# Kernel optimization log

Hardware: AMD Instinct MI355X
Metric: run time of the kernel (lower is better)

The kernel has to match this reference:

```python
import math
import jax, jax.numpy as jnp
import numpy as np

NUM_TOKENS = 8192
MODEL_DIM = 1024
NUM_EXPERTS = 64
CAPACITY_FACTOR = 1.0
MIN_CAPACITY = 8
SHIFT_PRIORITY = 0.5
LOAD_BALANCE_W = 0.01


def setup_inputs() -> dict:
    key = jax.random.key(0)
    k1, k2 = jax.random.split(key)
    x = jax.random.normal(k1, (NUM_TOKENS, MODEL_DIM), dtype=jnp.float32)
    # torch.nn.Linear(model_dim, num_experts, bias=False).weight -> [E, D]
    wg_weight = jax.random.normal(k2, (NUM_EXPERTS, MODEL_DIM), dtype=jnp.float32) * 0.02
    return {"x": x, "wg_weight": wg_weight}


def reference(x, wg_weight):
    S = x.shape[0]
    E = wg_weight.shape[0]
    # gate projection (fp32, as in DeepSpeed gating)
    logits = jnp.einsum('sd,ed->se', x, wg_weight)  # [S, E]
    gates = jax.nn.softmax(logits, axis=1)
    original_gates = gates

    # _capacity: ceil(S/E * capacity_factor), clamped to min_capacity (static)
    capacity = max(int(math.ceil(S / E * CAPACITY_FACTOR)), MIN_CAPACITY)

    indices1_s = jnp.argmax(gates, axis=1)                      # [S]
    mask1 = jax.nn.one_hot(indices1_s, E, dtype=jnp.int32)      # [S, E]
    exp_counts = jnp.sum(mask1, axis=0)                         # [E]

    # AuxLoss: GShard load-balance loss, zloss/entropy weights are 0
    me = jnp.mean(gates, axis=0)
    ce = jnp.mean(mask1.astype(gates.dtype), axis=0)
    l_aux = jnp.sum(me * ce) * E * LOAD_BALANCE_W

    # shifted-priority routing: sort tokens by -max_gate, roll, positional cumsum
    importance_scores = -jnp.max(gates, axis=1)                 # [S]
    sort_indices = jnp.argsort(importance_scores)               # [S]
    shift_num = int(S * SHIFT_PRIORITY)                         # static
    sort_indices = jnp.roll(sort_indices, shift_num)
    recover_indices = jnp.argsort(sort_indices)
    sorted_mask1 = mask1[sort_indices]                          # [S, E]
    sorted_cumsum1 = (jnp.cumsum(sorted_mask1, axis=0) - 1) * sorted_mask1
    locations1 = sorted_cumsum1[recover_indices]                # [S, E]

    # capacity dropping
    mask1 = mask1 * (locations1 < capacity).astype(jnp.int32)
    locations1_s = jnp.sum(locations1 * mask1, axis=1)          # [S]

    gates_masked = original_gates * mask1.astype(gates.dtype)   # [S, E]
    locations1_sc = jax.nn.one_hot(locations1_s, capacity, dtype=gates.dtype)  # [S, C]
    combine_weights = jnp.einsum('se,sc->sec', gates_masked, locations1_sc)    # [S, E, C]
    dispatch_mask = combine_weights.astype(bool)

    unrouted_token_rate = 1.0 - jnp.mean(jnp.any(dispatch_mask, axis=(-1, -2)).astype(jnp.float32))
    return l_aux, combine_weights, dispatch_mask, exp_counts, unrouted_token_rate
```

## Files before the change

### kernel.cpp

```cpp
#include <hip/hip_runtime.h>
#include <stdint.h>

#define S_TOK   8192
#define MODEL_D 1024
#define N_EXP   64
#define CAP     128
#define SHIFT   4096
#define SLAB    (N_EXP * CAP)
#define CDSIZE  ((size_t)S_TOK * SLAB)
#define OUT_FILL4 33554448


#define OFF_EXPERT   0
#define OFF_GATE     32768
#define OFF_KEY      65536
#define OFF_KEY2     98304
#define OFF_MEPART   163840
#define OFF_HIST     229376
#define OFF_DROP     294912
#define OFF_WGT      295936

__device__ __forceinline__ unsigned f2key(float f) {
    unsigned b = __float_as_uint(f);
    return (b & 0x80000000u) ? ~b : (b | 0x80000000u);
}

__global__ __launch_bounds__(256) void k_fill(float4* __restrict__ out4) {
    const float4 z = make_float4(0.f, 0.f, 0.f, 0.f);
    size_t i = (size_t)blockIdx.x * 256 + threadIdx.x;
    const size_t stride = (size_t)gridDim.x * 256;
    for (; i < OUT_FILL4; i += stride) out4[i] = z;
}

__global__ __launch_bounds__(256) void k0_repack(const float* __restrict__ wg,
                                                 float* __restrict__ wgT4) {
    int id0 = blockIdx.x * 256 + threadIdx.x;
#pragma unroll
    for (int i = 0; i < 4; ++i) {
        int id = id0 + i * 16384;
        int e = id >> 10;
        int d = id & 1023;
        wgT4[((d >> 2) * 64 + e) * 4 + (d & 3)] = wg[id];
    }
}

__global__ __launch_bounds__(256) void k1_gemm_softmax(
    const float* __restrict__ x, const float* __restrict__ wgT4,
    int* __restrict__ expert_id, float* __restrict__ gate1,
    unsigned* __restrict__ keys, float* __restrict__ me_part,
    int* __restrict__ hist_part)
{
    __shared__ float xs[32][256];
    __shared__ float lg[32][65];
    __shared__ float mrow[32], zrow[32];
    __shared__ int   exrow[32];
    __shared__ int   hist[64];
    __shared__ float mep[4][64];

    const int tid  = threadIdx.x;
    const int lane = tid & 63;
    const int wv   = tid >> 6;
    const int tok0 = blockIdx.x * 32;

    const float4* xg  = (const float4*)x;
    const float4* wg4 = (const float4*)wgT4;

    float acc[8] = {0.f,0.f,0.f,0.f,0.f,0.f,0.f,0.f};

    for (int chunk = 0; chunk < 4; ++chunk) {
        __syncthreads();
#pragma unroll
        for (int i = 0; i < 8; ++i) {
            int linear = tid + 256 * i;
            int t  = linear >> 6;
            int c4 = linear & 63;
            ((float4*)xs)[t * 64 + c4] = xg[(size_t)(tok0 + t) * 256 + chunk * 64 + c4];
        }
        __syncthreads();

#pragma unroll 4
        for (int dd = 0; dd < 256; dd += 4) {
            int d = chunk * 256 + dd;
            float4 w = wg4[(d >> 2) * 64 + lane];
#pragma unroll
            for (int t = 0; t < 8; ++t) {
                float4 xv = *(const float4*)&xs[wv * 8 + t][dd];
                acc[t] = fmaf(xv.x, w.x, acc[t]);
                acc[t] = fmaf(xv.y, w.y, acc[t]);
                acc[t] = fmaf(xv.z, w.z, acc[t]);
                acc[t] = fmaf(xv.w, w.w, acc[t]);
            }
        }
    }
#pragma unroll
    for (int t = 0; t < 8; ++t) lg[wv * 8 + t][lane] = acc[t];
    __syncthreads();

    if (tid < 64) hist[tid] = 0;
    if (tid < 32) {
        const int t = tid;
        float m = lg[t][0]; int am = 0;
        for (int e = 1; e < 64; ++e) {
            float v = lg[t][e];
            if (v > m) { m = v; am = e; }
        }
        float z = 0.f;
        for (int e = 0; e < 64; ++e) z += expf(lg[t][e] - m);
        float rz = 1.0f / z;
        mrow[t] = m; zrow[t] = rz; exrow[t] = am;
        int sG = tok0 + t;
        expert_id[sG] = am;
        gate1[sG] = rz;
        keys[sG] = f2key(-rz);
    }
    __syncthreads();

    if (tid < 32) atomicAdd(&hist[exrow[tid]], 1);
    {
        const int e = tid & 63, tg = tid >> 6;
        float p = 0.f;
        for (int t = tg; t < 32; t += 4) p += expf(lg[t][e] - mrow[t]) * zrow[t];
        mep[tg][e] = p;
    }
    __syncthreads();

    if (tid < 64) {
        me_part[blockIdx.x * 64 + tid] = mep[0][tid] + mep[1][tid] + mep[2][tid] + mep[3][tid];
        hist_part[blockIdx.x * 64 + tid] = hist[tid];
    }
}

__global__ __launch_bounds__(256) void k2_rank(const unsigned* __restrict__ keys,
                                               const int* __restrict__ expert_id,
                                               unsigned* __restrict__ key2)
{
    __shared__ uint4 k4[2048];
    const int tid = threadIdx.x;
    const uint4* kg = (const uint4*)keys;
    for (int i = tid; i < 2048; i += 256) k4[i] = kg[i];
    __syncthreads();

    const int sl = tid >> 3, part = tid & 7;
    const int sG = blockIdx.x * 32 + sl;
    const unsigned myk = ((const unsigned*)k4)[sG];
    int cnt = 0;
    const int qbase = part * 256;
    for (int q = 0; q < 256; ++q) {
        int qq = (q + part) & 255;
        uint4 v = k4[qbase + qq];
        int j = (qbase + qq) * 4;
        cnt += (v.x < myk) || (v.x == myk && (j + 0) < sG);
        cnt += (v.y < myk) || (v.y == myk && (j + 1) < sG);
        cnt += (v.z < myk) || (v.z == myk && (j + 2) < sG);
        cnt += (v.w < myk) || (v.w == myk && (j + 3) < sG);
    }
    cnt += __shfl_down(cnt, 4);
    cnt += __shfl_down(cnt, 2);
    cnt += __shfl_down(cnt, 1);
    if (part == 0) {
        int pos = (cnt + SHIFT) & (S_TOK - 1);
        key2[sG] = ((unsigned)expert_id[sG] << 13) | (unsigned)pos;
    }
}

__global__ __launch_bounds__(256) void k3_loc_scatter(const unsigned* __restrict__ key2,
                                                      const float* __restrict__ gate1,
                                                      float* __restrict__ out,
                                                      int* __restrict__ drop_part)
{
    __shared__ uint4 k4[2048];
    __shared__ int dropc;
    const int tid = threadIdx.x;
    if (tid == 0) dropc = 0;
    const uint4* kg = (const uint4*)key2;
    for (int i = tid; i < 2048; i += 256) k4[i] = kg[i];
    __syncthreads();

    const int sl = tid >> 3, part = tid & 7;
    const int sG = blockIdx.x * 32 + sl;
    const unsigned myk = ((const unsigned*)k4)[sG];
    const unsigned lo = myk & ~8191u;
    int cnt = 0;
    const int qbase = part * 256;
    for (int q = 0; q < 256; ++q) {
        int qq = (q + part) & 255;
        uint4 v = k4[qbase + qq];
        cnt += (v.x >= lo) && (v.x < myk);
        cnt += (v.y >= lo) && (v.y < myk);
        cnt += (v.z >= lo) && (v.z < myk);
        cnt += (v.w >= lo) && (v.w < myk);
    }
    cnt += __shfl_down(cnt, 4);
    cnt += __shfl_down(cnt, 2);
    cnt += __shfl_down(cnt, 1);
    if (part == 0) {
        if (cnt >= CAP) {
            atomicAdd(&dropc, 1);
        } else {
            unsigned e = myk >> 13;
            size_t idx = 1 + (size_t)sG * SLAB + (size_t)e * CAP + (unsigned)cnt;
            out[idx] = gate1[sG];
            out[idx + CDSIZE] = 1.0f;
        }
    }
    __syncthreads();
    if (tid == 0) drop_part[blockIdx.x] = dropc;
}

__global__ __launch_bounds__(256) void k_final(const float* __restrict__ me_part,
                                               const int* __restrict__ hist_part,
                                               const int* __restrict__ drop_part,
                                               float* __restrict__ out)
{
    __shared__ float msum[4][64];
    __shared__ int   hsum[4][64];
    __shared__ float contrib[64];
    const int tid = threadIdx.x;
    const int e = tid & 63, qt = tid >> 6;
    float ms = 0.f; int hs = 0;
    for (int p = qt * 64; p < qt * 64 + 64; ++p) {
        ms += me_part[p * 64 + e];
        hs += hist_part[p * 64 + e];
    }
    msum[qt][e] = ms; hsum[qt][e] = hs;
    __syncthreads();
    if (tid < 64) {
        float m = msum[0][tid] + msum[1][tid] + msum[2][tid] + msum[3][tid];
        int   h = hsum[0][tid] + hsum[1][tid] + hsum[2][tid] + hsum[3][tid];
        out[1 + 2 * CDSIZE + tid] = (float)h;
        contrib[tid] = (m * (1.0f / S_TOK)) * ((float)h * (1.0f / S_TOK));
    }
    __syncthreads();
    if (tid == 0) {
        float sum = 0.f;
        for (int i = 0; i < 64; ++i) sum += contrib[i];
        out[0] = sum * (float)N_EXP * 0.01f;
        int dr = 0;
        for (int p = 0; p < 256; ++p) dr += drop_part[p];
        out[1 + 2 * CDSIZE + 64] = (float)dr * (1.0f / S_TOK);
    }
}

extern "C" void kernel_launch(void* const* d_in, const int* in_sizes, int n_in,
                              void* d_out, int out_size, void* d_ws, size_t ws_size,
                              hipStream_t stream) {
    (void)in_sizes; (void)n_in; (void)out_size; (void)ws_size;
    const float* x  = (const float*)d_in[0];
    const float* wg = (const float*)d_in[1];
    float* out = (float*)d_out;
    char* ws = (char*)d_ws;

    int*      expert_id = (int*)(ws + OFF_EXPERT);
    float*    gate1     = (float*)(ws + OFF_GATE);
    unsigned* keys      = (unsigned*)(ws + OFF_KEY);
    unsigned* key2      = (unsigned*)(ws + OFF_KEY2);
    float*    me_part   = (float*)(ws + OFF_MEPART);
    int*      hist_part = (int*)(ws + OFF_HIST);
    int*      drop_part = (int*)(ws + OFF_DROP);
    float*    wgT4      = (float*)(ws + OFF_WGT);

    hipLaunchKernelGGL(k_fill,          dim3(8192), dim3(256), 0, stream, (float4*)out);
    hipLaunchKernelGGL(k0_repack,       dim3(64),   dim3(256), 0, stream, wg, wgT4);
    hipLaunchKernelGGL(k1_gemm_softmax, dim3(256),  dim3(256), 0, stream, x, wgT4,
                       expert_id, gate1, keys, me_part, hist_part);
    hipLaunchKernelGGL(k2_rank,         dim3(256),  dim3(256), 0, stream, keys, expert_id, key2);
    hipLaunchKernelGGL(k3_loc_scatter,  dim3(256),  dim3(256), 0, stream, key2, gate1, out, drop_part);
    hipLaunchKernelGGL(k_final,         dim3(1),    dim3(256), 0, stream,
                       me_part, hist_part, drop_part, out);
}
```

Before: 796.5 us.

## Merge output zero-fill into GEMM launch and fold final reduction into rank kernel

The zero-fill of the large output buffer now runs in extra blocks of the GEMM kernel, so the memory-bound fill overlaps the gate projection instead of running as its own serial launch. The GEMM is retiled to 16 tokens per block over 512 blocks for more parallelism. The scalar reduction (l_aux, expert counts, drop rate) moves into an extra block of the rank kernel. The drop count is now computed analytically as the sum over experts of max(count minus capacity, 0), which removes the per-block drop counters and the separate final kernel. The fill is bandwidth-bound, so overlapping it mainly hides the GEMM and launch costs.

```diff
diff --git a/kernel.cpp b/kernel.cpp
--- a/kernel.cpp
+++ b/kernel.cpp
@@ -10,26 +10,21 @@
 #define CDSIZE  ((size_t)S_TOK * SLAB)
 #define OUT_FILL4 33554448
 
+#define GEMM_BLOCKS 512
+#define TPB         16
+
 
 #define OFF_EXPERT   0
 #define OFF_GATE     32768
 #define OFF_KEY      65536
 #define OFF_KEY2     98304
-#define OFF_MEPART   163840
-#define OFF_HIST     229376
-#define OFF_DROP     294912
-#define OFF_WGT      295936
+#define OFF_MEPART   131072
+#define OFF_HIST     262144
+#define OFF_WGT      393216
 
 __device__ __forceinline__ unsigned f2key(float f) {
     unsigned b = __float_as_uint(f);
     return (b & 0x80000000u) ? ~b : (b | 0x80000000u);
-}
-
-__global__ __launch_bounds__(256) void k_fill(float4* __restrict__ out4) {
-    const float4 z = make_float4(0.f, 0.f, 0.f, 0.f);
-    size_t i = (size_t)blockIdx.x * 256 + threadIdx.x;
-    const size_t stride = (size_t)gridDim.x * 256;
-    for (; i < OUT_FILL4; i += stride) out4[i] = z;
 }
 
 __global__ __launch_bounds__(256) void k0_repack(const float* __restrict__ wg,
@@ -44,33 +39,43 @@
     }
 }
 
-__global__ __launch_bounds__(256) void k1_gemm_softmax(
+__global__ __launch_bounds__(256) void k1_fill_gemm(
     const float* __restrict__ x, const float* __restrict__ wgT4,
+    float* __restrict__ out,
     int* __restrict__ expert_id, float* __restrict__ gate1,
     unsigned* __restrict__ keys, float* __restrict__ me_part,
     int* __restrict__ hist_part)
 {
-    __shared__ float xs[32][256];
-    __shared__ float lg[32][65];
-    __shared__ float mrow[32], zrow[32];
-    __shared__ int   exrow[32];
+    const int b = blockIdx.x;
+    if (b >= GEMM_BLOCKS) {
+        const float4 z = make_float4(0.f, 0.f, 0.f, 0.f);
+        float4* out4 = (float4*)out;
+        size_t i = (size_t)(b - GEMM_BLOCKS) * 256 + threadIdx.x;
+        for (; i < OUT_FILL4; i += (size_t)8192 * 256) out4[i] = z;
+        return;
+    }
+
+    __shared__ float xs[TPB][256];
+    __shared__ float lg[TPB][65];
+    __shared__ float mrow[TPB], zrow[TPB];
+    __shared__ int   exrow[TPB];
     __shared__ int   hist[64];
     __shared__ float mep[4][64];
 
     const int tid  = threadIdx.x;
     const int lane = tid & 63;
     const int wv   = tid >> 6;
-    const int tok0 = blockIdx.x * 32;
+    const int tok0 = b * TPB;
 
     const float4* xg  = (const float4*)x;
     const float4* wg4 = (const float4*)wgT4;
 
-    float acc[8] = {0.f,0.f,0.f,0.f,0.f,0.f,0.f,0.f};
+    float acc[4] = {0.f, 0.f, 0.f, 0.f};
 
     for (int chunk = 0; chunk < 4; ++chunk) {
         __syncthreads();
 #pragma unroll
-        for (int i = 0; i < 8; ++i) {
+        for (int i = 0; i < 4; ++i) {
             int linear = tid + 256 * i;
             int t  = linear >> 6;
             int c4 = linear & 63;
@@ -83,8 +88,8 @@
             int d = chunk * 256 + dd;
             float4 w = wg4[(d >> 2) * 64 + lane];
 #pragma unroll
-            for (int t = 0; t < 8; ++t) {
-                float4 xv = *(const float4*)&xs[wv * 8 + t][dd];
+            for (int t = 0; t < 4; ++t) {
+                float4 xv = *(const float4*)&xs[wv * 4 + t][dd];
                 acc[t] = fmaf(xv.x, w.x, acc[t]);
                 acc[t] = fmaf(xv.y, w.y, acc[t]);
                 acc[t] = fmaf(xv.z, w.z, acc[t]);
@@ -93,11 +98,11 @@
         }
     }
 #pragma unroll
-    for (int t = 0; t < 8; ++t) lg[wv * 8 + t][lane] = acc[t];
+    for (int t = 0; t < 4; ++t) lg[wv * 4 + t][lane] = acc[t];
     __syncthreads();
 
     if (tid < 64) hist[tid] = 0;
-    if (tid < 32) {
+    if (tid < TPB) {
         const int t = tid;
         float m = lg[t][0]; int am = 0;
         for (int e = 1; e < 64; ++e) {
@@ -115,27 +120,58 @@
     }
     __syncthreads();
 
-    if (tid < 32) atomicAdd(&hist[exrow[tid]], 1);
+    if (tid < TPB) atomicAdd(&hist[exrow[tid]], 1);
     {
         const int e = tid & 63, tg = tid >> 6;
         float p = 0.f;
-        for (int t = tg; t < 32; t += 4) p += expf(lg[t][e] - mrow[t]) * zrow[t];
+        for (int t = tg; t < TPB; t += 4) p += expf(lg[t][e] - mrow[t]) * zrow[t];
         mep[tg][e] = p;
     }
     __syncthreads();
 
     if (tid < 64) {
-        me_part[blockIdx.x * 64 + tid] = mep[0][tid] + mep[1][tid] + mep[2][tid] + mep[3][tid];
-        hist_part[blockIdx.x * 64 + tid] = hist[tid];
-    }
-}
-
-__global__ __launch_bounds__(256) void k2_rank(const unsigned* __restrict__ keys,
-                                               const int* __restrict__ expert_id,
-                                               unsigned* __restrict__ key2)
+        me_part[b * 64 + tid] = mep[0][tid] + mep[1][tid] + mep[2][tid] + mep[3][tid];
+        hist_part[b * 64 + tid] = hist[tid];
+    }
+}
+
+__global__ __launch_bounds__(256) void k2_rank_scalars(
+    const unsigned* __restrict__ keys, const int* __restrict__ expert_id,
+    const float* __restrict__ me_part, const int* __restrict__ hist_part,
+    unsigned* __restrict__ key2, float* __restrict__ out)
 {
+    const int tid = threadIdx.x;
+    if (blockIdx.x == 256) {
+        __shared__ float msum[4][64];
+        __shared__ int   hsum[4][64];
+        __shared__ float contrib[64];
+        __shared__ int   keep[64];
+        const int e = tid & 63, qt = tid >> 6;
+        float ms = 0.f; int hs = 0;
+        for (int p = qt * 128; p < qt * 128 + 128; ++p) {
+            ms += me_part[p * 64 + e];
+            hs += hist_part[p * 64 + e];
+        }
+        msum[qt][e] = ms; hsum[qt][e] = hs;
+        __syncthreads();
+        if (tid < 64) {
+            float m = msum[0][tid] + msum[1][tid] + msum[2][tid] + msum[3][tid];
+            int   h = hsum[0][tid] + hsum[1][tid] + hsum[2][tid] + hsum[3][tid];
+            out[1 + 2 * CDSIZE + tid] = (float)h;
+            contrib[tid] = (m * (1.0f / S_TOK)) * ((float)h * (1.0f / S_TOK));
+            keep[tid] = (h < CAP) ? h : CAP;
+        }
+        __syncthreads();
+        if (tid == 0) {
+            float sum = 0.f; int kept = 0;
+            for (int i = 0; i < 64; ++i) { sum += contrib[i]; kept += keep[i]; }
+            out[0] = sum * (float)N_EXP * 0.01f;
+            out[1 + 2 * CDSIZE + 64] = (float)(S_TOK - kept) * (1.0f / S_TOK);
+        }
+        return;
+    }
+
     __shared__ uint4 k4[2048];
-    const int tid = threadIdx.x;
     const uint4* kg = (const uint4*)keys;
     for (int i = tid; i < 2048; i += 256) k4[i] = kg[i];
     __syncthreads();
@@ -165,13 +201,10 @@
 
 __global__ __launch_bounds__(256) void k3_loc_scatter(const unsigned* __restrict__ key2,
                                                       const float* __restrict__ gate1,
-                                                      float* __restrict__ out,
-                                                      int* __restrict__ drop_part)
+                                                      float* __restrict__ out)
 {
     __shared__ uint4 k4[2048];
-    __shared__ int dropc;
     const int tid = threadIdx.x;
-    if (tid == 0) dropc = 0;
     const uint4* kg = (const uint4*)key2;
     for (int i = tid; i < 2048; i += 256) k4[i] = kg[i];
     __syncthreads();
@@ -193,51 +226,11 @@
     cnt += __shfl_down(cnt, 4);
     cnt += __shfl_down(cnt, 2);
     cnt += __shfl_down(cnt, 1);
-    if (part == 0) {
-        if (cnt >= CAP) {
-            atomicAdd(&dropc, 1);
-        } else {
-            unsigned e = myk >> 13;
-            size_t idx = 1 + (size_t)sG * SLAB + (size_t)e * CAP + (unsigned)cnt;
-            out[idx] = gate1[sG];
-            out[idx + CDSIZE] = 1.0f;
-        }
-    }
-    __syncthreads();
-    if (tid == 0) drop_part[blockIdx.x] = dropc;
-}
-
-__global__ __launch_bounds__(256) void k_final(const float* __restrict__ me_part,
-                                               const int* __restrict__ hist_part,
-                                               const int* __restrict__ drop_part,
-                                               float* __restrict__ out)
-{
-    __shared__ float msum[4][64];
-    __shared__ int   hsum[4][64];
-    __shared__ float contrib[64];
-    const int tid = threadIdx.x;
-    const int e = tid & 63, qt = tid >> 6;
-    float ms = 0.f; int hs = 0;
-    for (int p = qt * 64; p < qt * 64 + 64; ++p) {
-        ms += me_part[p * 64 + e];
-        hs += hist_part[p * 64 + e];
-    }
-    msum[qt][e] = ms; hsum[qt][e] = hs;
-    __syncthreads();
-    if (tid < 64) {
-        float m = msum[0][tid] + msum[1][tid] + msum[2][tid] + msum[3][tid];
-        int   h = hsum[0][tid] + hsum[1][tid] + hsum[2][tid] + hsum[3][tid];
-        out[1 + 2 * CDSIZE + tid] = (float)h;
-        contrib[tid] = (m * (1.0f / S_TOK)) * ((float)h * (1.0f / S_TOK));
-    }
-    __syncthreads();
-    if (tid == 0) {
-        float sum = 0.f;
-        for (int i = 0; i < 64; ++i) sum += contrib[i];
-        out[0] = sum * (float)N_EXP * 0.01f;
-        int dr = 0;
-        for (int p = 0; p < 256; ++p) dr += drop_part[p];
-        out[1 + 2 * CDSIZE + 64] = (float)dr * (1.0f / S_TOK);
+    if (part == 0 && cnt < CAP) {
+        unsigned e = myk >> 13;
+        size_t idx = 1 + (size_t)sG * SLAB + (size_t)e * CAP + (unsigned)cnt;
+        out[idx] = gate1[sG];
+        out[idx + CDSIZE] = 1.0f;
     }
 }
 
@@ -256,15 +249,13 @@
     unsigned* key2      = (unsigned*)(ws + OFF_KEY2);
     float*    me_part   = (float*)(ws + OFF_MEPART);
     int*      hist_part = (int*)(ws + OFF_HIST);
-    int*      drop_part = (int*)(ws + OFF_DROP);
     float*    wgT4      = (float*)(ws + OFF_WGT);
 
-    hipLaunchKernelGGL(k_fill,          dim3(8192), dim3(256), 0, stream, (float4*)out);
-    hipLaunchKernelGGL(k0_repack,       dim3(64),   dim3(256), 0, stream, wg, wgT4);
-    hipLaunchKernelGGL(k1_gemm_softmax, dim3(256),  dim3(256), 0, stream, x, wgT4,
-                       expert_id, gate1, keys, me_part, hist_part);
-    hipLaunchKernelGGL(k2_rank,         dim3(256),  dim3(256), 0, stream, keys, expert_id, key2);
-    hipLaunchKernelGGL(k3_loc_scatter,  dim3(256),  dim3(256), 0, stream, key2, gate1, out, drop_part);
-    hipLaunchKernelGGL(k_final,         dim3(1),    dim3(256), 0, stream,
-                       me_part, hist_part, drop_part, out);
-}
+    hipLaunchKernelGGL(k0_repack,       dim3(64),                dim3(256), 0, stream, wg, wgT4);
+    hipLaunchKernelGGL(k1_fill_gemm,    dim3(GEMM_BLOCKS + 8192), dim3(256), 0, stream,
+                       x, wgT4, out, expert_id, gate1, keys, me_part, hist_part);
+    hipLaunchKernelGGL(k2_rank_scalars, dim3(257),               dim3(256), 0, stream,
+                       keys, expert_id, me_part, hist_part, key2, out);
+    hipLaunchKernelGGL(k3_loc_scatter,  dim3(256),               dim3(256), 0, stream,
+                       key2, gate1, out);
+}
```

After: 714.3 us. 10.3% less time.
